# Kernel optimization log

Measured on AMD Instinct MI355X. Metric: run time of the kernel, lower is better.

## Reference

```python
import jax, jax.numpy as jnp
import numpy as np

N = 500000
D = 128
R = D // 4  # reduction = 4
G = 2048    # number of graphs


def setup_inputs() -> dict:
    key = jax.random.key(0)
    ks = jax.random.split(key, 8)
    x = jax.random.normal(ks[0], (N, D), dtype=jnp.float32)
    batch = jnp.sort(jax.random.randint(ks[1], (N,), 0, G))
    # SE-gate MLP params (nn.Linear stores weight as [out,in]; we store transposed for x @ W)
    fc_w1 = jax.random.normal(ks[2], (D, R), dtype=jnp.float32) * (1.0 / np.sqrt(D))
    fc_b1 = jnp.zeros((R,), dtype=jnp.float32)
    fc_w2 = jax.random.normal(ks[3], (R, D), dtype=jnp.float32) * (1.0 / np.sqrt(R))
    fc_b2 = jnp.zeros((D,), dtype=jnp.float32)
    # xavier-uniform weight_matrix [D, D]
    lim = np.sqrt(6.0 / (D + D))
    W = jax.random.uniform(ks[4], (D, D), dtype=jnp.float32, minval=-lim, maxval=lim)
    return {"x": x, "batch": batch, "size": G,
            "fc_w1": fc_w1, "fc_b1": fc_b1, "fc_w2": fc_w2, "fc_b2": fc_b2, "W": W}


def reference(x, batch, size, fc_w1, fc_b1, fc_w2, fc_b2, W):
    # gated SE-block: attention = tanh(MLP(x)); x = attention*x + x
    attention = jnp.tanh(jnp.maximum(x @ fc_w1 + fc_b1, 0.0) @ fc_w2 + fc_b2)
    x2 = attention * x + x  # [N, D]
    # global_mean_pool: segment mean over graphs
    seg_sum = jax.ops.segment_sum(x2, batch, num_segments=size)           # [G, D]
    counts = jax.ops.segment_sum(jnp.ones((x2.shape[0],), x2.dtype), batch, num_segments=size)
    mean = seg_sum / jnp.maximum(counts, 1.0)[:, None]                     # [G, D]
    transformed_global = jnp.tanh(mean @ W)                                # [G, D]
    # gather-broadcast per-graph global back to nodes, per-node attention coef
    coefs = jax.nn.sigmoid(jnp.sum(x2 * transformed_global[batch], axis=1))  # [N]
    weighted = coefs[:, None] * x2                                          # [N, D]
    return jax.ops.segment_sum(weighted, batch, num_segments=size)          # [G, D]
```

## Files before the change

kernel.cpp:

```cpp
#include <hip/hip_runtime.h>

#define DDIM 128
#define RDIM 32
#define BLK  256
#define XSTR 136
#define HSTR 40

typedef __attribute__((ext_vector_type(8))) short bf16x8;
typedef __attribute__((ext_vector_type(4))) float f32x4;

__device__ __forceinline__ float tanh_fast(float v) {
  float e = __expf(2.f * v);
  return 1.f - 2.f / (e + 1.f);
}
__device__ __forceinline__ float sigmoid_fast(float v) {
  return 1.f / (1.f + __expf(-v));
}
__device__ __forceinline__ unsigned short f2bf(float f) {
  unsigned u = __float_as_uint(f);
  u += 0x7fffu + ((u >> 16) & 1u);
  return (unsigned short)(u >> 16);
}
__device__ __forceinline__ float bf2f(unsigned short s) {
  return __uint_as_float(((unsigned)s) << 16);
}
__device__ __forceinline__ int lower_bound(const int* __restrict__ b, int n, int v) {
  int lo = 0, hi = n;
  while (lo < hi) { int m = (lo + hi) >> 1; if (b[m] < v) lo = m + 1; else hi = m; }
  return lo;
}

__global__ void k0_prep(const float* __restrict__ w1, const float* __restrict__ w2,
                        unsigned short* __restrict__ w1f, unsigned short* __restrict__ w2f)
{
  const int i  = blockIdx.x * blockDim.x + threadIdx.x;
  const int l  = i & 63;
  const int lr = l & 15, lq = l >> 4;
  if (i < 512) {
    const int frag = i >> 6;
    const int nt = frag >> 2, kk = frag & 3;
    const int col = nt * 16 + lr;
    const int kb  = kk * 32 + lq * 8;
    bf16x8 v;
    #pragma unroll
    for (int j = 0; j < 8; ++j) v[j] = (short)f2bf(w1[(kb + j) * RDIM + col]);
    *(bf16x8*)&w1f[(size_t)i * 8] = v;
  } else {
    const int frag = (i - 512) >> 6;
    const int col = frag * 16 + lr;
    const int kb  = lq * 8;
    bf16x8 v;
    #pragma unroll
    for (int j = 0; j < 8; ++j) v[j] = (short)f2bf(w2[(kb + j) * DDIM + col]);
    *(bf16x8*)&w2f[(size_t)(i - 512) * 8] = v;
  }
}

__global__ __launch_bounds__(BLK, 3) void k1_mfma(
    const float* __restrict__ x,
    const unsigned short* __restrict__ w1f, const float* __restrict__ b1,
    const unsigned short* __restrict__ w2f, const float* __restrict__ b2,
    unsigned short* __restrict__ x2, int N)
{
  __shared__ unsigned short xs4[4][16 * XSTR];
  __shared__ unsigned short hs4[4][16 * HSTR];

  const int t  = threadIdx.x;
  const int l  = t & 63;
  const int wv = t >> 6;
  const int lr = l & 15;
  const int lq = l >> 4;
  const int node0 = (blockIdx.x * 4 + wv) * 16;
  if (node0 >= N) return;
  unsigned short* xs = xs4[wv];
  unsigned short* hs = hs4[wv];

  bf16x8 w1r[2][4], w2r[8];
  #pragma unroll
  for (int nt = 0; nt < 2; ++nt)
    #pragma unroll
    for (int kk = 0; kk < 4; ++kk)
      w1r[nt][kk] = *(const bf16x8*)&w1f[(size_t)((nt * 4 + kk) * 64 + l) * 8];
  #pragma unroll
  for (int nt = 0; nt < 8; ++nt)
    w2r[nt] = *(const bf16x8*)&w2f[(size_t)(nt * 64 + l) * 8];

  float b1v[2], b2v[8];
  b1v[0] = b1[lr]; b1v[1] = b1[16 + lr];
  #pragma unroll
  for (int nt = 0; nt < 8; ++nt) b2v[nt] = b2[nt * 16 + lr];

  #pragma unroll
  for (int j = 0; j < 8; ++j) {
    int i = l + j * 64;
    int node = i >> 5, c4 = (i & 31) << 2;
    float4 v = make_float4(0.f, 0.f, 0.f, 0.f);
    if (node0 + node < N) v = *(const float4*)&x[(size_t)(node0 + node) * DDIM + c4];
    ushort4 o;
    o.x = f2bf(v.x); o.y = f2bf(v.y); o.z = f2bf(v.z); o.w = f2bf(v.w);
    *(ushort4*)&xs[node * XSTR + c4] = o;
  }

  f32x4 hacc[2];
  #pragma unroll
  for (int nt = 0; nt < 2; ++nt)
    #pragma unroll
    for (int c = 0; c < 4; ++c) hacc[nt][c] = b1v[nt];

  #pragma unroll
  for (int kk = 0; kk < 4; ++kk) {
    bf16x8 a = *(const bf16x8*)&xs[lr * XSTR + kk * 32 + lq * 8];
    hacc[0] = __builtin_amdgcn_mfma_f32_16x16x32_bf16(a, w1r[0][kk], hacc[0], 0, 0, 0);
    hacc[1] = __builtin_amdgcn_mfma_f32_16x16x32_bf16(a, w1r[1][kk], hacc[1], 0, 0, 0);
  }

  #pragma unroll
  for (int nt = 0; nt < 2; ++nt)
    #pragma unroll
    for (int c = 0; c < 4; ++c)
      hs[(lq * 4 + c) * HSTR + nt * 16 + lr] = f2bf(fmaxf(hacc[nt][c], 0.f));

  bf16x8 ah = *(const bf16x8*)&hs[lr * HSTR + lq * 8];
  f32x4 cacc[8];
  #pragma unroll
  for (int nt = 0; nt < 8; ++nt)
    #pragma unroll
    for (int c = 0; c < 4; ++c) cacc[nt][c] = b2v[nt];
  #pragma unroll
  for (int nt = 0; nt < 8; ++nt)
    cacc[nt] = __builtin_amdgcn_mfma_f32_16x16x32_bf16(ah, w2r[nt], cacc[nt], 0, 0, 0);

  #pragma unroll
  for (int nt = 0; nt < 8; ++nt)
    #pragma unroll
    for (int c = 0; c < 4; ++c) {
      int m   = lq * 4 + c;
      int col = nt * 16 + lr;
      int off = m * XSTR + col;
      float a  = tanh_fast(cacc[nt][c]);
      float xv = bf2f(xs[off]);
      xs[off]  = f2bf(xv * (1.f + a));
    }

  #pragma unroll
  for (int k = 0; k < 4; ++k) {
    int idx  = l + k * 64;
    int node = idx >> 4, coff = (idx & 15) * 8;
    if (node0 + node < N)
      *(bf16x8*)&x2[(size_t)(node0 + node) * DDIM + coff] =
          *(const bf16x8*)&xs[node * XSTR + coff];
  }
}

__global__ void k3_graph(
    const unsigned short* __restrict__ x2, const int* __restrict__ batch,
    const float* __restrict__ W, float* __restrict__ out, int N)
{
  __shared__ __align__(16) float part[8][132];
  __shared__ float meanv[DDIM];
  __shared__ float tgs[DDIM];
  __shared__ int bounds[2];
  const int g = blockIdx.x, t = threadIdx.x;
  if (t == 0) bounds[0] = lower_bound(batch, N, g);
  if (t == 1) bounds[1] = lower_bound(batch, N, g + 1);
  __syncthreads();
  const int lo = bounds[0], hi = bounds[1];
  const int q = t & 31, s = t >> 5;

  {
    float acc[4] = {0.f, 0.f, 0.f, 0.f};
    for (int n = lo + s; n < hi; n += 8) {
      ushort4 u = *(const ushort4*)&x2[(size_t)n * DDIM + q * 4];
      acc[0] += bf2f(u.x); acc[1] += bf2f(u.y); acc[2] += bf2f(u.z); acc[3] += bf2f(u.w);
    }
    *(float4*)&part[s][q * 4] = make_float4(acc[0], acc[1], acc[2], acc[3]);
  }
  __syncthreads();
  if (t < DDIM) {
    float m = 0.f;
    #pragma unroll
    for (int s2 = 0; s2 < 8; ++s2) m += part[s2][t];
    float invc = (hi > lo) ? 1.f / (float)(hi - lo) : 0.f;
    meanv[t] = m * invc;
  }
  __syncthreads();

  if (t < DDIM) {
    float a = 0.f;
    #pragma unroll 8
    for (int k = 0; k < DDIM; ++k) a = fmaf(meanv[k], W[k * DDIM + t], a);
    tgs[t] = tanh_fast(a);
  }
  __syncthreads();

  float4 tg4 = *(const float4*)&tgs[q * 4];
  float tga[4] = {tg4.x, tg4.y, tg4.z, tg4.w};
  float acc[4] = {0.f, 0.f, 0.f, 0.f};
  for (int n = lo + s; n < hi; n += 8) {
    ushort4 u = *(const ushort4*)&x2[(size_t)n * DDIM + q * 4];
    float xv[4] = {bf2f(u.x), bf2f(u.y), bf2f(u.z), bf2f(u.w)};
    float p = xv[0] * tga[0] + xv[1] * tga[1] + xv[2] * tga[2] + xv[3] * tga[3];
    #pragma unroll
    for (int off = 16; off >= 1; off >>= 1) p += __shfl_xor(p, off, 64);
    float coef = sigmoid_fast(p);
    #pragma unroll
    for (int c = 0; c < 4; ++c) acc[c] = fmaf(coef, xv[c], acc[c]);
  }
  *(float4*)&part[s][q * 4] = make_float4(acc[0], acc[1], acc[2], acc[3]);
  __syncthreads();

  if (t < DDIM) {
    float m = 0.f;
    #pragma unroll
    for (int s2 = 0; s2 < 8; ++s2) m += part[s2][t];
    out[(size_t)g * DDIM + t] = m;
  }
}

extern "C" void kernel_launch(void* const* d_in, const int* in_sizes, int n_in,
                              void* d_out, int out_size, void* d_ws, size_t ws_size,
                              hipStream_t stream) {
  const float* x     = (const float*)d_in[0];
  const int*   batch = (const int*)d_in[1];
  const float* w1 = (const float*)d_in[3];
  const float* b1 = (const float*)d_in[4];
  const float* w2 = (const float*)d_in[5];
  const float* b2 = (const float*)d_in[6];
  const float* W  = (const float*)d_in[7];
  float* out = (float*)d_out;

  const int N = in_sizes[0] / DDIM;
  const int G = out_size / DDIM;

  unsigned short* w1f = (unsigned short*)d_ws;
  unsigned short* w2f = w1f + 4096;
  unsigned short* x2  = w2f + 4096;
  (void)ws_size; (void)n_in;

  hipLaunchKernelGGL(k0_prep, dim3(4), dim3(BLK), 0, stream, w1, w2, w1f, w2f);
  const int grid1 = (N + 63) / 64;
  hipLaunchKernelGGL(k1_mfma, dim3(grid1), dim3(BLK), 0, stream, x, w1f, b1, w2f, b2, x2, N);
  hipLaunchKernelGGL(k3_graph, dim3(G), dim3(BLK), 0, stream, x2, batch, W, out, N);
}
```

Baseline: 154.2 us.

## Make k1 waves persistent over multiple tiles with register-prefetched input

Each wave of the SE-gate kernel now handles 10 consecutive 16-node tiles instead of one, so the weight-fragment and bias register loads are amortized over more work. The next tile's fp32 input is loaded into registers while the current tile goes through the MFMA and tanh stages, overlapping global loads with compute. The bf16 conversion now uses packed hip_bfloat162 intrinsics. The costs are a tenfold smaller grid, roughly 780 blocks, which may underfill the GPU, and higher register pressure from the prefetch buffer.

Result: slower. 211.4 us (+37.1%).

```diff
diff --git a/kernel.cpp b/kernel.cpp
--- a/kernel.cpp
+++ b/kernel.cpp
@@ -1,10 +1,12 @@
 #include <hip/hip_runtime.h>
+#include <hip/hip_bf16.h>
 
 #define DDIM 128
 #define RDIM 32
 #define BLK  256
 #define XSTR 136
 #define HSTR 40
+#define TPW  10
 
 typedef __attribute__((ext_vector_type(8))) short bf16x8;
 typedef __attribute__((ext_vector_type(4))) float f32x4;
@@ -23,6 +25,10 @@
 }
 __device__ __forceinline__ float bf2f(unsigned short s) {
   return __uint_as_float(((unsigned)s) << 16);
+}
+__device__ __forceinline__ unsigned pkbf(float lo, float hi) {
+  __hip_bfloat162 t2 = __float22bfloat162_rn(make_float2(lo, hi));
+  return *reinterpret_cast<unsigned*>(&t2);
 }
 __device__ __forceinline__ int lower_bound(const int* __restrict__ b, int n, int v) {
   int lo = 0, hi = n;
@@ -70,8 +76,9 @@
   const int wv = t >> 6;
   const int lr = l & 15;
   const int lq = l >> 4;
-  const int node0 = (blockIdx.x * 4 + wv) * 16;
-  if (node0 >= N) return;
+  const long gw  = (long)blockIdx.x * 4 + wv;
+  const long tb0 = gw * (TPW * 16);
+  if (tb0 >= N) return;
   unsigned short* xs = xs4[wv];
   unsigned short* hs = hs4[wv];
 
@@ -90,65 +97,89 @@
   #pragma unroll
   for (int nt = 0; nt < 8; ++nt) b2v[nt] = b2[nt * 16 + lr];
 
+  const int snode = l >> 5;
+  const int scol  = (l & 31) * 4;
+
+  float4 buf[8];
   #pragma unroll
   for (int j = 0; j < 8; ++j) {
-    int i = l + j * 64;
-    int node = i >> 5, c4 = (i & 31) << 2;
-    float4 v = make_float4(0.f, 0.f, 0.f, 0.f);
-    if (node0 + node < N) v = *(const float4*)&x[(size_t)(node0 + node) * DDIM + c4];
-    ushort4 o;
-    o.x = f2bf(v.x); o.y = f2bf(v.y); o.z = f2bf(v.z); o.w = f2bf(v.w);
-    *(ushort4*)&xs[node * XSTR + c4] = o;
-  }
-
-  f32x4 hacc[2];
-  #pragma unroll
-  for (int nt = 0; nt < 2; ++nt)
-    #pragma unroll
-    for (int c = 0; c < 4; ++c) hacc[nt][c] = b1v[nt];
-
-  #pragma unroll
-  for (int kk = 0; kk < 4; ++kk) {
-    bf16x8 a = *(const bf16x8*)&xs[lr * XSTR + kk * 32 + lq * 8];
-    hacc[0] = __builtin_amdgcn_mfma_f32_16x16x32_bf16(a, w1r[0][kk], hacc[0], 0, 0, 0);
-    hacc[1] = __builtin_amdgcn_mfma_f32_16x16x32_bf16(a, w1r[1][kk], hacc[1], 0, 0, 0);
-  }
-
-  #pragma unroll
-  for (int nt = 0; nt < 2; ++nt)
-    #pragma unroll
-    for (int c = 0; c < 4; ++c)
-      hs[(lq * 4 + c) * HSTR + nt * 16 + lr] = f2bf(fmaxf(hacc[nt][c], 0.f));
-
-  bf16x8 ah = *(const bf16x8*)&hs[lr * HSTR + lq * 8];
-  f32x4 cacc[8];
-  #pragma unroll
-  for (int nt = 0; nt < 8; ++nt)
-    #pragma unroll
-    for (int c = 0; c < 4; ++c) cacc[nt][c] = b2v[nt];
-  #pragma unroll
-  for (int nt = 0; nt < 8; ++nt)
-    cacc[nt] = __builtin_amdgcn_mfma_f32_16x16x32_bf16(ah, w2r[nt], cacc[nt], 0, 0, 0);
-
-  #pragma unroll
-  for (int nt = 0; nt < 8; ++nt)
-    #pragma unroll
-    for (int c = 0; c < 4; ++c) {
-      int m   = lq * 4 + c;
-      int col = nt * 16 + lr;
-      int off = m * XSTR + col;
-      float a  = tanh_fast(cacc[nt][c]);
-      float xv = bf2f(xs[off]);
-      xs[off]  = f2bf(xv * (1.f + a));
-    }
-
-  #pragma unroll
-  for (int k = 0; k < 4; ++k) {
-    int idx  = l + k * 64;
-    int node = idx >> 4, coff = (idx & 15) * 8;
-    if (node0 + node < N)
-      *(bf16x8*)&x2[(size_t)(node0 + node) * DDIM + coff] =
-          *(const bf16x8*)&xs[node * XSTR + coff];
+    long node = tb0 + snode + 2 * j;
+    buf[j] = (node < N) ? *(const float4*)&x[(size_t)node * DDIM + scol]
+                        : make_float4(0.f, 0.f, 0.f, 0.f);
+  }
+
+  for (int tt = 0; tt < TPW; ++tt) {
+    const long tb = tb0 + (long)tt * 16;
+    if (tb >= N) break;
+
+    #pragma unroll
+    for (int j = 0; j < 8; ++j) {
+      int node = snode + 2 * j;
+      uint2 pk;
+      pk.x = pkbf(buf[j].x, buf[j].y);
+      pk.y = pkbf(buf[j].z, buf[j].w);
+      *(uint2*)&xs[node * XSTR + scol] = pk;
+    }
+
+    if (tt + 1 < TPW) {
+      const long tbn = tb + 16;
+      #pragma unroll
+      for (int j = 0; j < 8; ++j) {
+        long node = tbn + snode + 2 * j;
+        buf[j] = (node < N) ? *(const float4*)&x[(size_t)node * DDIM + scol]
+                            : make_float4(0.f, 0.f, 0.f, 0.f);
+      }
+    }
+
+    f32x4 hacc[2];
+    #pragma unroll
+    for (int nt = 0; nt < 2; ++nt)
+      #pragma unroll
+      for (int c = 0; c < 4; ++c) hacc[nt][c] = b1v[nt];
+
+    #pragma unroll
+    for (int kk = 0; kk < 4; ++kk) {
+      bf16x8 a = *(const bf16x8*)&xs[lr * XSTR + kk * 32 + lq * 8];
+      hacc[0] = __builtin_amdgcn_mfma_f32_16x16x32_bf16(a, w1r[0][kk], hacc[0], 0, 0, 0);
+      hacc[1] = __builtin_amdgcn_mfma_f32_16x16x32_bf16(a, w1r[1][kk], hacc[1], 0, 0, 0);
+    }
+
+    #pragma unroll
+    for (int nt = 0; nt < 2; ++nt)
+      #pragma unroll
+      for (int c = 0; c < 4; ++c)
+        hs[(lq * 4 + c) * HSTR + nt * 16 + lr] = f2bf(fmaxf(hacc[nt][c], 0.f));
+
+    bf16x8 ah = *(const bf16x8*)&hs[lr * HSTR + lq * 8];
+    f32x4 cacc[8];
+    #pragma unroll
+    for (int nt = 0; nt < 8; ++nt)
+      #pragma unroll
+      for (int c = 0; c < 4; ++c) cacc[nt][c] = b2v[nt];
+    #pragma unroll
+    for (int nt = 0; nt < 8; ++nt)
+      cacc[nt] = __builtin_amdgcn_mfma_f32_16x16x32_bf16(ah, w2r[nt], cacc[nt], 0, 0, 0);
+
+    #pragma unroll
+    for (int nt = 0; nt < 8; ++nt)
+      #pragma unroll
+      for (int c = 0; c < 4; ++c) {
+        int m   = lq * 4 + c;
+        int col = nt * 16 + lr;
+        int off = m * XSTR + col;
+        float a  = tanh_fast(cacc[nt][c]);
+        float xv = bf2f(xs[off]);
+        xs[off]  = f2bf(xv * (1.f + a));
+      }
+
+    #pragma unroll
+    for (int k = 0; k < 4; ++k) {
+      int idx  = l + k * 64;
+      int node = idx >> 4, coff = (idx & 15) * 8;
+      if (tb + node < N)
+        *(bf16x8*)&x2[(size_t)(tb + node) * DDIM + coff] =
+            *(const bf16x8*)&xs[node * XSTR + coff];
+    }
   }
 }
 
@@ -238,7 +269,8 @@
   (void)ws_size; (void)n_in;
 
   hipLaunchKernelGGL(k0_prep, dim3(4), dim3(BLK), 0, stream, w1, w2, w1f, w2f);
-  const int grid1 = (N + 63) / 64;
+  const int nodes_per_block = 64 * TPW;
+  const int grid1 = (N + nodes_per_block - 1) / nodes_per_block;
   hipLaunchKernelGGL(k1_mfma, dim3(grid1), dim3(BLK), 0, stream, x, w1f, b1, w2f, b2, x2, N);
   hipLaunchKernelGGL(k3_graph, dim3(G), dim3(BLK), 0, stream, x2, batch, W, out, N);
 }
```

## Compute transposed MFMA products so x stays in registers, staging weights in LDS

Applied to the files above, without the earlier changes.

Swaps the MFMA operand order so each lane owns one node row and consumes x straight from global memory in registers. This removes the per-wave LDS staging tile for x and the read-modify-write of the gated result in LDS. Weight fragments are now copied into shared memory once per block instead of being held in registers, and bf16 packing uses the paired conversion intrinsic. The cost is that x is read from global twice per lane (an fp32 copy and a bf16 fragment copy), a block-wide barrier is added, and row-per-lane stores are less coalesced.

Result: slower. 164.1 us (+6.4%).

```diff
diff --git a/kernel.cpp b/kernel.cpp
--- a/kernel.cpp
+++ b/kernel.cpp
@@ -1,9 +1,9 @@
 #include <hip/hip_runtime.h>
+#include <hip/hip_bf16.h>
 
 #define DDIM 128
 #define RDIM 32
 #define BLK  256
-#define XSTR 136
 #define HSTR 40
 
 typedef __attribute__((ext_vector_type(8))) short bf16x8;
@@ -24,6 +24,10 @@
 __device__ __forceinline__ float bf2f(unsigned short s) {
   return __uint_as_float(((unsigned)s) << 16);
 }
+__device__ __forceinline__ unsigned pkbf(float lo, float hi) {
+  __hip_bfloat162 t2 = __float22bfloat162_rn(make_float2(lo, hi));
+  return *reinterpret_cast<unsigned*>(&t2);
+}
 __device__ __forceinline__ int lower_bound(const int* __restrict__ b, int n, int v) {
   int lo = 0, hi = n;
   while (lo < hi) { int m = (lo + hi) >> 1; if (b[m] < v) lo = m + 1; else hi = m; }
@@ -31,124 +35,121 @@
 }
 
 __global__ void k0_prep(const float* __restrict__ w1, const float* __restrict__ w2,
-                        unsigned short* __restrict__ w1f, unsigned short* __restrict__ w2f)
+                        unsigned short* __restrict__ w1tf, unsigned short* __restrict__ w2tf)
 {
   const int i  = blockIdx.x * blockDim.x + threadIdx.x;
   const int l  = i & 63;
-  const int lr = l & 15, lq = l >> 4;
+  const int lr = l & 15, q = l >> 4;
   if (i < 512) {
     const int frag = i >> 6;
-    const int nt = frag >> 2, kk = frag & 3;
-    const int col = nt * 16 + lr;
-    const int kb  = kk * 32 + lq * 8;
+    const int mt2 = frag >> 2, kk = frag & 3;
     bf16x8 v;
     #pragma unroll
-    for (int j = 0; j < 8; ++j) v[j] = (short)f2bf(w1[(kb + j) * RDIM + col]);
-    *(bf16x8*)&w1f[(size_t)i * 8] = v;
+    for (int j = 0; j < 8; ++j)
+      v[j] = (short)f2bf(w1[(size_t)(kk * 32 + q * 8 + j) * RDIM + mt2 * 16 + lr]);
+    *(bf16x8*)&w1tf[(size_t)i * 8] = v;
   } else {
-    const int frag = (i - 512) >> 6;
-    const int col = frag * 16 + lr;
-    const int kb  = lq * 8;
+    const int mt = (i - 512) >> 6;
     bf16x8 v;
     #pragma unroll
-    for (int j = 0; j < 8; ++j) v[j] = (short)f2bf(w2[(kb + j) * DDIM + col]);
-    *(bf16x8*)&w2f[(size_t)(i - 512) * 8] = v;
+    for (int j = 0; j < 8; ++j)
+      v[j] = (short)f2bf(w2[(size_t)(q * 8 + j) * DDIM + mt * 16 + lr]);
+    *(bf16x8*)&w2tf[(size_t)(i - 512) * 8] = v;
   }
 }
 
 __global__ __launch_bounds__(BLK, 3) void k1_mfma(
     const float* __restrict__ x,
-    const unsigned short* __restrict__ w1f, const float* __restrict__ b1,
-    const unsigned short* __restrict__ w2f, const float* __restrict__ b2,
+    const unsigned short* __restrict__ w1tf, const float* __restrict__ b1,
+    const unsigned short* __restrict__ w2tf, const float* __restrict__ b2,
     unsigned short* __restrict__ x2, int N)
 {
-  __shared__ unsigned short xs4[4][16 * XSTR];
+  __shared__ unsigned short w1t[512 * 8];
+  __shared__ unsigned short w2t[512 * 8];
   __shared__ unsigned short hs4[4][16 * HSTR];
 
   const int t  = threadIdx.x;
   const int l  = t & 63;
   const int wv = t >> 6;
   const int lr = l & 15;
-  const int lq = l >> 4;
+  const int q  = l >> 4;
+
+  for (int i = t; i < 512; i += BLK) {
+    ((bf16x8*)w1t)[i] = ((const bf16x8*)w1tf)[i];
+    ((bf16x8*)w2t)[i] = ((const bf16x8*)w2tf)[i];
+  }
+  __syncthreads();
+
   const int node0 = (blockIdx.x * 4 + wv) * 16;
   if (node0 >= N) return;
-  unsigned short* xs = xs4[wv];
+  const int row  = node0 + lr;
+  const int rowc = min(row, N - 1);
+  const float* xrow = x + (size_t)rowc * DDIM;
+
+  float4 xg[8];
+  #pragma unroll
+  for (int mt = 0; mt < 8; ++mt)
+    xg[mt] = *(const float4*)(xrow + mt * 16 + q * 4);
+
+  bf16x8 xf[4];
+  #pragma unroll
+  for (int kk = 0; kk < 4; ++kk) {
+    float4 a = *(const float4*)(xrow + kk * 32 + q * 8);
+    float4 b = *(const float4*)(xrow + kk * 32 + q * 8 + 4);
+    uint4 u;
+    u.x = pkbf(a.x, a.y); u.y = pkbf(a.z, a.w);
+    u.z = pkbf(b.x, b.y); u.w = pkbf(b.z, b.w);
+    xf[kk] = *(bf16x8*)&u;
+  }
+
+  f32x4 hacc[2];
+  #pragma unroll
+  for (int mt2 = 0; mt2 < 2; ++mt2) {
+    float4 bv = *(const float4*)(b1 + mt2 * 16 + q * 4);
+    hacc[mt2][0] = bv.x; hacc[mt2][1] = bv.y; hacc[mt2][2] = bv.z; hacc[mt2][3] = bv.w;
+  }
+  #pragma unroll
+  for (int kk = 0; kk < 4; ++kk) {
+    #pragma unroll
+    for (int mt2 = 0; mt2 < 2; ++mt2) {
+      bf16x8 wfr = *(const bf16x8*)&w1t[(size_t)((mt2 * 4 + kk) * 64 + l) * 8];
+      hacc[mt2] = __builtin_amdgcn_mfma_f32_16x16x32_bf16(wfr, xf[kk], hacc[mt2], 0, 0, 0);
+    }
+  }
+
   unsigned short* hs = hs4[wv];
-
-  bf16x8 w1r[2][4], w2r[8];
-  #pragma unroll
-  for (int nt = 0; nt < 2; ++nt)
-    #pragma unroll
-    for (int kk = 0; kk < 4; ++kk)
-      w1r[nt][kk] = *(const bf16x8*)&w1f[(size_t)((nt * 4 + kk) * 64 + l) * 8];
-  #pragma unroll
-  for (int nt = 0; nt < 8; ++nt)
-    w2r[nt] = *(const bf16x8*)&w2f[(size_t)(nt * 64 + l) * 8];
-
-  float b1v[2], b2v[8];
-  b1v[0] = b1[lr]; b1v[1] = b1[16 + lr];
-  #pragma unroll
-  for (int nt = 0; nt < 8; ++nt) b2v[nt] = b2[nt * 16 + lr];
-
-  #pragma unroll
-  for (int j = 0; j < 8; ++j) {
-    int i = l + j * 64;
-    int node = i >> 5, c4 = (i & 31) << 2;
-    float4 v = make_float4(0.f, 0.f, 0.f, 0.f);
-    if (node0 + node < N) v = *(const float4*)&x[(size_t)(node0 + node) * DDIM + c4];
-    ushort4 o;
-    o.x = f2bf(v.x); o.y = f2bf(v.y); o.z = f2bf(v.z); o.w = f2bf(v.w);
-    *(ushort4*)&xs[node * XSTR + c4] = o;
-  }
-
-  f32x4 hacc[2];
-  #pragma unroll
-  for (int nt = 0; nt < 2; ++nt)
-    #pragma unroll
-    for (int c = 0; c < 4; ++c) hacc[nt][c] = b1v[nt];
-
-  #pragma unroll
-  for (int kk = 0; kk < 4; ++kk) {
-    bf16x8 a = *(const bf16x8*)&xs[lr * XSTR + kk * 32 + lq * 8];
-    hacc[0] = __builtin_amdgcn_mfma_f32_16x16x32_bf16(a, w1r[0][kk], hacc[0], 0, 0, 0);
-    hacc[1] = __builtin_amdgcn_mfma_f32_16x16x32_bf16(a, w1r[1][kk], hacc[1], 0, 0, 0);
-  }
-
-  #pragma unroll
-  for (int nt = 0; nt < 2; ++nt)
-    #pragma unroll
-    for (int c = 0; c < 4; ++c)
-      hs[(lq * 4 + c) * HSTR + nt * 16 + lr] = f2bf(fmaxf(hacc[nt][c], 0.f));
-
-  bf16x8 ah = *(const bf16x8*)&hs[lr * HSTR + lq * 8];
+  #pragma unroll
+  for (int mt2 = 0; mt2 < 2; ++mt2) {
+    float h0 = fmaxf(hacc[mt2][0], 0.f), h1 = fmaxf(hacc[mt2][1], 0.f);
+    float h2 = fmaxf(hacc[mt2][2], 0.f), h3 = fmaxf(hacc[mt2][3], 0.f);
+    uint2 p; p.x = pkbf(h0, h1); p.y = pkbf(h2, h3);
+    *(uint2*)&hs[lr * HSTR + mt2 * 16 + q * 4] = p;
+  }
+  bf16x8 ah = *(const bf16x8*)&hs[lr * HSTR + q * 8];
+
   f32x4 cacc[8];
   #pragma unroll
-  for (int nt = 0; nt < 8; ++nt)
-    #pragma unroll
-    for (int c = 0; c < 4; ++c) cacc[nt][c] = b2v[nt];
-  #pragma unroll
-  for (int nt = 0; nt < 8; ++nt)
-    cacc[nt] = __builtin_amdgcn_mfma_f32_16x16x32_bf16(ah, w2r[nt], cacc[nt], 0, 0, 0);
-
-  #pragma unroll
-  for (int nt = 0; nt < 8; ++nt)
-    #pragma unroll
-    for (int c = 0; c < 4; ++c) {
-      int m   = lq * 4 + c;
-      int col = nt * 16 + lr;
-      int off = m * XSTR + col;
-      float a  = tanh_fast(cacc[nt][c]);
-      float xv = bf2f(xs[off]);
-      xs[off]  = f2bf(xv * (1.f + a));
+  for (int mt = 0; mt < 8; ++mt)
+    #pragma unroll
+    for (int c = 0; c < 4; ++c) cacc[mt][c] = 0.f;
+  #pragma unroll
+  for (int mt = 0; mt < 8; ++mt) {
+    bf16x8 wfr = *(const bf16x8*)&w2t[(size_t)(mt * 64 + l) * 8];
+    cacc[mt] = __builtin_amdgcn_mfma_f32_16x16x32_bf16(wfr, ah, cacc[mt], 0, 0, 0);
+  }
+
+  if (row < N) {
+    unsigned short* orow = x2 + (size_t)row * DDIM;
+    #pragma unroll
+    for (int mt = 0; mt < 8; ++mt) {
+      float4 bv = *(const float4*)(b2 + mt * 16 + q * 4);
+      float y0 = xg[mt].x * (1.f + tanh_fast(cacc[mt][0] + bv.x));
+      float y1 = xg[mt].y * (1.f + tanh_fast(cacc[mt][1] + bv.y));
+      float y2 = xg[mt].z * (1.f + tanh_fast(cacc[mt][2] + bv.z));
+      float y3 = xg[mt].w * (1.f + tanh_fast(cacc[mt][3] + bv.w));
+      uint2 p; p.x = pkbf(y0, y1); p.y = pkbf(y2, y3);
+      *(uint2*)&orow[mt * 16 + q * 4] = p;
     }
-
-  #pragma unroll
-  for (int k = 0; k < 4; ++k) {
-    int idx  = l + k * 64;
-    int node = idx >> 4, coff = (idx & 15) * 8;
-    if (node0 + node < N)
-      *(bf16x8*)&x2[(size_t)(node0 + node) * DDIM + coff] =
-          *(const bf16x8*)&xs[node * XSTR + coff];
   }
 }
 
@@ -232,13 +233,13 @@
   const int N = in_sizes[0] / DDIM;
   const int G = out_size / DDIM;
 
-  unsigned short* w1f = (unsigned short*)d_ws;
-  unsigned short* w2f = w1f + 4096;
-  unsigned short* x2  = w2f + 4096;
+  unsigned short* w1tf = (unsigned short*)d_ws;
+  unsigned short* w2tf = w1tf + 4096;
+  unsigned short* x2   = w2tf + 4096;
   (void)ws_size; (void)n_in;
 
-  hipLaunchKernelGGL(k0_prep, dim3(4), dim3(BLK), 0, stream, w1, w2, w1f, w2f);
+  hipLaunchKernelGGL(k0_prep, dim3(4), dim3(BLK), 0, stream, w1, w2, w1tf, w2tf);
   const int grid1 = (N + 63) / 64;
-  hipLaunchKernelGGL(k1_mfma, dim3(grid1), dim3(BLK), 0, stream, x, w1f, b1, w2f, b2, x2, N);
+  hipLaunchKernelGGL(k1_mfma, dim3(grid1), dim3(BLK), 0, stream, x, w1tf, b1, w2tf, b2, x2, N);
   hipLaunchKernelGGL(k3_graph, dim3(G), dim3(BLK), 0, stream, x2, batch, W, out, N);
 }
```
